# Performance work log

Measured on AMD Instinct MI355X. Metric: run time of the kernel, lower is better.

The kernel has to match this reference:

```python
import jax, jax.numpy as jnp
import numpy as np

NUM_GRAPHS = 1024
NODES_PER_GRAPH = 128
NUM_EDGES = 1048576
D_IN = 128          # n_heads * head_out_feats = input/concat dim
ATT_HEADS = 2       # intra/inter GATConv(d, 32, 2) as in HDN-DDI repo
ATT_OUT = 32
POOL_HEADS = 2      # pool = GATConv(128, 64, 2)
POOL_OUT = 64
EPS = 1e-5          # PyG LayerNorm eps


def _segment_softmax(e, seg, n):
    # numerically-stable softmax over edges grouped by destination node
    m = jax.ops.segment_max(e, seg, num_segments=n)
    m = jnp.where(jnp.isfinite(m), m, 0.0)
    p = jnp.exp(e - m[seg])
    s = jax.ops.segment_sum(p, seg, num_segments=n)
    return p / (s[seg] + 1e-16)


def _gat(x_src, x_dst, edge_index, w_src, w_dst, att_src, att_dst, bias, self_loops):
    # PyG GATConv: linear -> per-head attention logits -> leaky_relu(0.2) ->
    # softmax over incoming edges -> weighted sum of source features -> concat heads + bias
    H, C = att_src.shape
    nd = x_dst.shape[0]
    hs = (x_src @ w_src).reshape(-1, H, C)   # [Ns,H,C]
    hd = (x_dst @ w_dst).reshape(-1, H, C)   # [Nd,H,C]
    a_s = jnp.einsum('nhc,hc->nh', hs, att_src)
    a_d = jnp.einsum('nhc,hc->nh', hd, att_dst)
    src, dst = edge_index[0], edge_index[1]
    if self_loops:  # PyG default add_self_loops=True (non-bipartite case)
        loop = jnp.arange(nd)
        src = jnp.concatenate([src, loop])
        dst = jnp.concatenate([dst, loop])
    e = jax.nn.leaky_relu(a_s[src] + a_d[dst], 0.2)  # [E,H]
    alpha = _segment_softmax(e, dst, nd)
    out = jax.ops.segment_sum(hs[src] * alpha[:, :, None], dst, num_segments=nd)
    return out.reshape(nd, H * C) + bias


def _graph_layernorm(x, batch, weight, bias, n_graphs):
    # PyG LayerNorm(mode='graph'): normalize over all nodes+channels of each graph
    f = x.shape[-1]
    cnt = jax.ops.segment_sum(jnp.ones((x.shape[0],), x.dtype), batch, num_segments=n_graphs)
    norm = jnp.maximum(cnt, 1.0) * f
    mean = jax.ops.segment_sum(x.sum(-1), batch, num_segments=n_graphs) / norm
    xc = x - mean[batch][:, None]
    var = jax.ops.segment_sum((xc * xc).sum(-1), batch, num_segments=n_graphs) / norm
    return (xc / jnp.sqrt(var + EPS)[batch][:, None]) * weight + bias


def setup_inputs() -> dict:
    key = jax.random.key(0)
    ks = jax.random.split(key, 24)
    B, P, E, D = NUM_GRAPHS, NODES_PER_GRAPH, NUM_EDGES, D_IN
    N = B * P

    def intra_edges(k):  # within-graph edges, no self-loops
        k1, k2, k3 = jax.random.split(k, 3)
        g = jax.random.randint(k1, (E,), 0, B)
        s = jax.random.randint(k2, (E,), 0, P)
        d = (s + 1 + jax.random.randint(k3, (E,), 0, P - 1)) % P
        return jnp.stack([g * P + s, g * P + d])

    def inter_edges(k):  # bipartite head-node -> tail-node edges within same graph pair
        k1, k2, k3 = jax.random.split(k, 3)
        g = jax.random.randint(k1, (E,), 0, B)
        s = jax.random.randint(k2, (E,), 0, P)
        d = jax.random.randint(k3, (E,), 0, P)
        return jnp.stack([g * P + s, g * P + d])

    batch = jnp.repeat(jnp.arange(B), P)
    # one global supernode (type 2) per graph: the last node
    y = jnp.tile(jnp.concatenate([jnp.zeros((P - 1,), jnp.int32), jnp.array([2], jnp.int32)]), B)
    p = lambda k, shape: jax.random.normal(k, shape, jnp.float32) * 0.1
    return {
        'h_x': jax.random.normal(ks[0], (N, D), jnp.float32),
        't_x': jax.random.normal(ks[1], (N, D), jnp.float32),
        'h_edge_index': intra_edges(ks[2]),
        't_edge_index': intra_edges(ks[3]),
        'b_edge_index': inter_edges(ks[4]),
        'h_batch': batch,
        't_batch': batch,
        'h_y': y,
        't_y': y,
        'w_intra': p(ks[5], (D, ATT_HEADS * ATT_OUT)),
        'att_intra_src': p(ks[6], (ATT_HEADS, ATT_OUT)),
        'att_intra_dst': p(ks[7], (ATT_HEADS, ATT_OUT)),
        'b_intra': jnp.zeros((ATT_HEADS * ATT_OUT,), jnp.float32),
        'w_inter_src': p(ks[8], (D, ATT_HEADS * ATT_OUT)),
        'w_inter_dst': p(ks[9], (D, ATT_HEADS * ATT_OUT)),
        'att_inter_src': p(ks[10], (ATT_HEADS, ATT_OUT)),
        'att_inter_dst': p(ks[11], (ATT_HEADS, ATT_OUT)),
        'b_inter': jnp.zeros((ATT_HEADS * ATT_OUT,), jnp.float32),
        'w_pool': p(ks[12], (D, POOL_HEADS * POOL_OUT)),
        'att_pool_src': p(ks[13], (POOL_HEADS, POOL_OUT)),
        'att_pool_dst': p(ks[14], (POOL_HEADS, POOL_OUT)),
        'b_pool': jnp.zeros((POOL_HEADS * POOL_OUT,), jnp.float32),
        'ln_weight': jnp.ones((D,), jnp.float32),
        'ln_bias': jnp.zeros((D,), jnp.float32),
    }


def reference(h_x, t_x, h_edge_index, t_edge_index, b_edge_index, h_batch, t_batch, h_y, t_y,
              w_intra, att_intra_src, att_intra_dst, b_intra,
              w_inter_src, w_inter_dst, att_inter_src, att_inter_dst, b_inter,
              w_pool, att_pool_src, att_pool_dst, b_pool, ln_weight, ln_bias):
    h_in = jax.nn.elu(h_x)
    t_in = jax.nn.elu(t_x)
    # intra-graph attention (shared GATConv applied to both drug graphs)
    h_intra = _gat(h_in, h_in, h_edge_index, w_intra, w_intra, att_intra_src, att_intra_dst, b_intra, True)
    t_intra = _gat(t_in, t_in, t_edge_index, w_intra, w_intra, att_intra_src, att_intra_dst, b_intra, True)
    # inter-graph (bipartite) attention: h->t and reversed t->h with shared weights
    t_inter = _gat(h_in, t_in, b_edge_index, w_inter_src, w_inter_dst, att_inter_src, att_inter_dst, b_inter, False)
    h_inter = _gat(t_in, h_in, b_edge_index[::-1], w_inter_src, w_inter_dst, att_inter_src, att_inter_dst, b_inter, False)
    h_rep = jnp.concatenate([h_intra, h_inter], 1)  # [N, 128]
    t_rep = jnp.concatenate([t_intra, t_inter], 1)
    h_nx = jax.nn.elu(_graph_layernorm(h_rep, h_batch, ln_weight, ln_bias, NUM_GRAPHS))
    t_nx = jax.nn.elu(_graph_layernorm(t_rep, t_batch, ln_weight, ln_bias, NUM_GRAPHS))
    h_out = _gat(h_nx, h_nx, h_edge_index, w_pool, w_pool, att_pool_src, att_pool_dst, b_pool, True)
    t_out = _gat(t_nx, t_nx, t_edge_index, w_pool, w_pool, att_pool_src, att_pool_dst, b_pool, True)
    # get_node: gather the single type-2 supernode per graph (exactly NUM_GRAPHS of them)
    h_idx = jnp.where(h_y == 2, size=NUM_GRAPHS)[0]
    t_idx = jnp.where(t_y == 2, size=NUM_GRAPHS)[0]
    return h_out, t_out, h_out[h_idx], t_out[t_idx]
```

## Files before the change

kernel.cpp:

```cpp
#include <hip/hip_runtime.h>
#include <hip/hip_bf16.h>

#define NN 131072
#define NG 1024
#define NE 1048576
#define EB 16384
#define NB 64

typedef __hip_bfloat16 bf16;
typedef __attribute__((ext_vector_type(8))) short short8v;
typedef __attribute__((ext_vector_type(4))) float f32x4;

__device__ __forceinline__ float b2f(bf16 v){ return __bfloat162float(v); }
__device__ __forceinline__ bf16 f2b(float v){ return __float2bfloat16(v); }
__device__ __forceinline__ unsigned short f2bu(float v){ bf16 b = f2b(v); return *(unsigned short*)&b; }
__device__ __forceinline__ float eluf(float x){ return x > 0.f ? x : expm1f(x); }
__device__ __forceinline__ float lrelu(float x){ return x >= 0.f ? x : 0.2f*x; }

__device__ __forceinline__ float ldx(const void* p, size_t i, int f){
  return f ? ((const float*)p)[i] : b2f(((const bf16*)p)[i]);
}

struct EPtrs { const int *s0,*d0,*s1,*d1,*s2,*d2,*s3,*d3; };

__global__ void detect_dtype(const unsigned short* __restrict__ x, int* __restrict__ flag){
  if (blockIdx.x==0 && threadIdx.x==0){
    int bad = 0;
    for (int i=0;i<2048;i++){
      unsigned short e = (x[i] >> 7) & 0xFF;
      if (e == 0xFF) bad++;
      else if (e >= 0x90) bad++;
      else if (e != 0 && e < 0x60) bad++;
    }
    *flag = (bad > 64) ? 1 : 0;
  }
}

__global__ __launch_bounds__(256) void hist_bagg(EPtrs ep, int* __restrict__ Hb){
  __shared__ int cnt[NG];
  int set = blockIdx.y, blk = blockIdx.x, t = threadIdx.x;
  const int* dp = set==0 ? ep.d0 : set==1 ? ep.d1 : set==2 ? ep.d2 : ep.d3;
  for (int i=t;i<NG;i+=256) cnt[i]=0;
  __syncthreads();
  int e0 = blk*EB;
  for (int i=t;i<EB;i+=256) atomicAdd(&cnt[dp[e0+i]>>7],1);
  __syncthreads();
  for (int i=t;i<NG;i+=256) Hb[((size_t)set*NB+blk)*NG+i] = cnt[i];
}

__global__ __launch_bounds__(1024) void scan_bagg(const int* __restrict__ Hb, int* __restrict__ Bb,
                                                  int* __restrict__ base_gs){
  __shared__ int sh[1024];
  int set = blockIdx.x, t = threadIdx.x;
  int run = 0;
  for (int b=0;b<NB;b++){
    int v = Hb[((size_t)set*NB + b)*NG + t];
    Bb[((size_t)set*NB + b)*NG + t] = run;
    run += v;
  }
  int val = run; sh[t] = run; __syncthreads();
  for (int d=1; d<1024; d<<=1){
    int add = (t>=d)? sh[t-d] : 0; __syncthreads();
    val += add; sh[t] = val; __syncthreads();
  }
  int binbase = val - run;
  base_gs[set*(NG+1) + t] = binbase;
  if (t==1023) base_gs[set*(NG+1)+NG] = val;
  for (int b=0;b<NB;b++) Bb[((size_t)set*NB + b)*NG + t] += binbase;
}

__global__ __launch_bounds__(256) void scatter_bagg(EPtrs ep, const int* __restrict__ Bb,
                                                    unsigned short* __restrict__ pk){
  __shared__ int cur[NG];
  int set = blockIdx.y, blk = blockIdx.x, t = threadIdx.x;
  const int* sp = set==0 ? ep.s0 : set==1 ? ep.s1 : set==2 ? ep.s2 : ep.s3;
  const int* dp = set==0 ? ep.d0 : set==1 ? ep.d1 : set==2 ? ep.d2 : ep.d3;
  for (int i=t;i<NG;i+=256) cur[i] = Bb[((size_t)set*NB+blk)*NG+i];
  __syncthreads();
  int e0 = blk*EB;
  for (int i=t;i<EB;i+=256){
    int e = e0+i;
    int d = dp[e], s = sp[e];
    int p = atomicAdd(&cur[d>>7],1);
    pk[(size_t)set*NE + p] = (unsigned short)(((d & 127) << 8) | (s & 127));
  }
}

__global__ __launch_bounds__(256) void prep_kernel(
    const void* w_intra, const void* w_isrc, const void* w_idst, const void* att_xd, const void* w_pool,
    const void* att_is, const void* att_id, const void* att_xs,
    const void* att_ps, const void* att_pd,
    const void* b_intra, const void* b_inter, const void* b_pool,
    const void* ln_w, const void* ln_b,
    bf16* __restrict__ Wtc, bf16* __restrict__ Wtp, float* __restrict__ vdst, float* __restrict__ sm,
    const int* __restrict__ fp){
  int f = *fp;
  int t = threadIdx.x;
  for (int i=t; i<16384; i+=256){
    int j = i & 7, l = (i>>3) & 63, ks = (i>>9) & 3, nt = i >> 11;
    int k = ks*32 + ((l>>4)<<3) + j;
    int c = nt*16 + (l & 15);
    float w1 = (c < 64) ? ldx(w_intra, k*64 + c, f) : ldx(w_isrc, k*64 + (c-64), f);
    Wtc[i] = f2b(w1);
    Wtp[i] = f2b(ldx(w_pool, k*128 + c, f));
  }
  {
    int k = t>>1, h = t&1; float a = 0.f;
    for (int c=0;c<32;c++) a += ldx(w_idst, k*64 + h*32 + c, f) * ldx(att_xd, h*32 + c, f);
    vdst[t] = a;
  }
  if (t < 64){
    sm[t]     = ldx(att_is, t, f);
    sm[64+t]  = ldx(att_id, t, f);
    sm[128+t] = ldx(att_xs, t, f);
    sm[448+t] = ldx(b_intra, t, f);
    sm[512+t] = ldx(b_inter, t, f);
  }
  if (t < 128){
    sm[192+t] = ldx(att_ps, t, f);
    sm[320+t] = ldx(att_pd, t, f);
    sm[576+t] = ldx(b_pool, t, f);
    sm[704+t] = ldx(ln_w, t, f);
    sm[832+t] = ldx(ln_b, t, f);
  }
}

template<int MODE>
__global__ __launch_bounds__(256) void gemm_fused(const void* A, const bf16* __restrict__ Wt, bf16* __restrict__ C,
    const int* __restrict__ fp, const int* __restrict__ fsel, size_t aoff_bf, size_t aoff_f32,
    const float* __restrict__ vdst,
    const float* __restrict__ attA, const float* __restrict__ attB, const float* __restrict__ attC,
    float* __restrict__ oS, float* __restrict__ oD, float* __restrict__ oX, float* __restrict__ oDx){
  constexpr bool ELU = (MODE==0);
  const bf16* Ab = (const bf16*)A + ((fp == nullptr && fsel && *fsel) ? aoff_f32 : aoff_bf);
  int tid = threadIdx.x;
  int w = tid >> 6, l = tid & 63;
  int lr = l & 15, lg = l >> 4;
  size_t row = (size_t)blockIdx.x*64 + w*16 + lr;
  int f = fp ? *fp : 0;
  f32x4 acc[8];
  #pragma unroll
  for (int nt=0;nt<8;nt++) acc[nt] = (f32x4){0.f,0.f,0.f,0.f};
  float dx0 = 0.f, dx1 = 0.f;
  #pragma unroll
  for (int ks=0;ks<4;ks++){
    short8v af;
    size_t ab = row*128 + ks*32 + lg*8;
    if (fp){
      if (f){
        const float* Af = (const float*)A;
        #pragma unroll
        for (int j=0;j<8;j++){
          float v = Af[ab+j]; if (ELU) v = eluf(v);
          if constexpr (MODE==0){ int k = ks*32+lg*8+j; dx0 += v*vdst[k*2]; dx1 += v*vdst[k*2+1]; }
          ((unsigned short*)&af)[j] = f2bu(v);
        }
      } else {
        const unsigned short* Au = (const unsigned short*)A;
        short8v raw = *(const short8v*)(Au + ab);
        #pragma unroll
        for (int j=0;j<8;j++){
          bf16 b; *(unsigned short*)&b = ((unsigned short*)&raw)[j];
          float v = b2f(b); if (ELU) v = eluf(v);
          if constexpr (MODE==0){ int k = ks*32+lg*8+j; dx0 += v*vdst[k*2]; dx1 += v*vdst[k*2+1]; }
          ((unsigned short*)&af)[j] = f2bu(v);
        }
      }
    } else {
      af = *(const short8v*)((const unsigned short*)Ab + ab);
    }
    #pragma unroll
    for (int nt=0;nt<8;nt++){
      short8v bfr = *(const short8v*)((const unsigned short*)Wt + (size_t)((nt*4+ks)*64 + l)*8);
      acc[nt] = __builtin_amdgcn_mfma_f32_16x16x32_bf16(af, bfr, acc[nt], 0, 0, 0);
    }
  }
  if constexpr (MODE==0){
    dx0 += __shfl_xor(dx0, 16); dx0 += __shfl_xor(dx0, 32);
    dx1 += __shfl_xor(dx1, 16); dx1 += __shfl_xor(dx1, 32);
    if (lg == 0){ oDx[row*2] = dx0; oDx[row*2+1] = dx1; }
  }
  size_t crow = (size_t)blockIdx.x*64 + w*16 + lg*4;
  #pragma unroll
  for (int nt=0;nt<8;nt++)
    #pragma unroll
    for (int r=0;r<4;r++)
      C[(crow + r)*128 + nt*16 + lr] = f2b(acc[nt][r]);
  #pragma unroll
  for (int rg=0; rg<4; ++rg){
    float pS0=0.f,pS1=0.f,pD0=0.f,pD1=0.f,pX0=0.f,pX1=0.f;
    #pragma unroll
    for (int nt=0;nt<8;nt++){
      float v = acc[nt][rg];
      int c = nt*16 + lr;
      if constexpr (MODE==0){
        if (nt<4){
          float a=attA[c], b=attB[c];
          if (nt<2){ pS0+=v*a; pD0+=v*b; } else { pS1+=v*a; pD1+=v*b; }
        } else {
          float xw=attC[c-64];
          if (nt<6) pX0+=v*xw; else pX1+=v*xw;
        }
      } else {
        float a=attA[c], b=attB[c];
        if (nt<4){ pS0+=v*a; pD0+=v*b; } else { pS1+=v*a; pD1+=v*b; }
      }
    }
    #pragma unroll
    for (int o=1;o<16;o<<=1){
      pS0+=__shfl_xor(pS0,o); pS1+=__shfl_xor(pS1,o);
      pD0+=__shfl_xor(pD0,o); pD1+=__shfl_xor(pD1,o);
      if constexpr (MODE==0){ pX0+=__shfl_xor(pX0,o); pX1+=__shfl_xor(pX1,o); }
    }
    if (lr == 0){
      size_t n = crow + rg;
      oS[n*2]=pS0; oS[n*2+1]=pS1;
      oD[n*2]=pD0; oD[n*2+1]=pD1;
      if constexpr (MODE==0){ oX[n*2]=pX0; oX[n*2+1]=pX1; }
    }
  }
}

struct GatSet {
  const unsigned short* pk;
  const int* gb;
  const bf16* F;
  const float* aS;
  const float* aD;
  const float* bias;
  int col_in;
  int self_loops;
  int col_off;
  int pad;
  size_t obase_bf, obase_f32, gbase;
};
struct GatSet4 { GatSet s[4]; };

template<int FD>
__global__ __launch_bounds__(512) void gat_mfma(GatSet4 sets, void* out,
    const int* __restrict__ fp, const int* __restrict__ fsel){
  constexpr int NH = FD/2;
  constexpr int NT = NH/16;
  constexpr int KSH = (FD==64)?5:6;
  __shared__ bf16 Pm[128*128];
  __shared__ bf16 Ft[NH*128];
  __shared__ unsigned int Msh[128*16];
  __shared__ float aS0[128], aS1[128], aD0[128], aD1[128], rsum[128];
  const GatSet S = sets.s[blockIdx.y];
  int fo = fp ? *fp : -1;
  size_t obase = (fsel && *fsel) ? S.obase_f32 : S.obase_bf;
  int g = blockIdx.x, t = threadIdx.x;

  if (t < 128){
    float2 v = ((const float2*)S.aS)[g*128+t]; aS0[t]=v.x; aS1[t]=v.y;
    float2 d = ((const float2*)S.aD)[g*128+t]; aD0[t]=d.x; aD1[t]=d.y;
  }
  for (int i=t;i<2048;i+=512) Msh[i]=0;
  __syncthreads();

  {
    int gbeg = S.gb[g], gend = S.gb[g+1];
    for (int i=gbeg+t; i<gend; i+=512){
      unsigned v = S.pk[i];
      unsigned r = v>>8, s = v&127;
      atomicAdd(&Msh[r*16 + (s>>3)], 1u<<((s&7)*4));
    }
    if (S.self_loops && t<128) atomicAdd(&Msh[t*16 + (t>>3)], 1u<<((t&7)*4));
  }
  {
    const unsigned short* Fu = (const unsigned short*)S.F;
    unsigned short* FtU = (unsigned short*)Ft;
    for (int i=t; i<NH*128; i+=512){
      int c = i & (NH-1), k = i >> KSH;
      FtU[c*128 + (k ^ (8*(c&7)))] = Fu[((size_t)(g*128+k))*128 + S.col_in + c];
    }
  }
  __syncthreads();

  int w = t >> 6, l = t & 63, lr = l & 15, lg = l >> 4;
  int r = t >> 2, q = t & 3;

  #pragma unroll
  for (int h=0; h<2; ++h){
    if (h == 1){
      const unsigned short* Fu = (const unsigned short*)S.F;
      unsigned short* FtU = (unsigned short*)Ft;
      for (int i=t; i<NH*128; i+=512){
        int c = i & (NH-1), k = i >> KSH;
        FtU[c*128 + (k ^ (8*(c&7)))] = Fu[((size_t)(g*128+k))*128 + S.col_in + NH + c];
      }
    }
    {
      float ad = h ? aD1[r] : aD0[r];
      const float* aSh = h ? aS1 : aS0;
      float rs = 0.f;
      unsigned int* PmW = (unsigned int*)Pm;
      int dbase = r*64, sw = 4*(r&7);
      unsigned mw = 0;
      #pragma unroll
      for (int i=0;i<16;i++){
        int c = q*32 + 2*i;
        if ((i&3)==0) mw = Msh[r*16 + (c>>3)];
        float m0 = (float)((mw >> ((c&7)*4)) & 15u);
        float m1 = (float)((mw >> (((c&7)+1)*4)) & 15u);
        float p0 = m0 * __expf(lrelu(aSh[c]   + ad));
        float p1 = m1 * __expf(lrelu(aSh[c+1] + ad));
        rs += p0 + p1;
        PmW[dbase + ((q*16+i) ^ sw)] = (unsigned)f2bu(p0) | ((unsigned)f2bu(p1)<<16);
      }
      rs += __shfl_xor(rs,1); rs += __shfl_xor(rs,2);
      if (q==0) rsum[r] = rs;
    }
    __syncthreads();
    f32x4 acc[NT];
    #pragma unroll
    for (int nt=0;nt<NT;nt++) acc[nt] = (f32x4){0.f,0.f,0.f,0.f};
    const unsigned short* PmU = (const unsigned short*)Pm;
    const unsigned short* FtU = (const unsigned short*)Ft;
    int arow = w*16 + lr;
    #pragma unroll
    for (int ks=0;ks<4;ks++){
      short8v af = *(const short8v*)(PmU + arow*128 + ((ks*32+lg*8) ^ (8*(arow&7))));
      #pragma unroll
      for (int nt=0;nt<NT;nt++){
        int brow = nt*16 + lr;
        short8v bfr = *(const short8v*)(FtU + brow*128 + ((ks*32+lg*8) ^ (8*(brow&7))));
        acc[nt] = __builtin_amdgcn_mfma_f32_16x16x32_bf16(af, bfr, acc[nt], 0, 0, 0);
      }
    }
    #pragma unroll
    for (int rg=0; rg<4; ++rg){
      int rrow = w*16 + lg*4 + rg;
      float rinv = 1.f / (rsum[rrow] + 1e-16f);
      int n = g*128 + rrow;
      bool gw = (fp != nullptr) && (rrow == 127);
      #pragma unroll
      for (int nt=0;nt<NT;nt++){
        int c = h*NH + nt*16 + lr;
        float o = acc[nt][rg]*rinv + S.bias[c];
        size_t oi = obase + (size_t)n*128 + S.col_off + c;
        if (fo > 0){
          ((float*)out)[oi] = o;
          if (gw) ((float*)out)[S.gbase + (size_t)g*128 + c] = o;
        } else {
          ((bf16*)out)[oi] = f2b(o);
          if (gw) ((bf16*)out)[S.gbase + (size_t)g*128 + c] = f2b(o);
        }
      }
    }
    __syncthreads();
  }
}

__global__ __launch_bounds__(512) void graph_ln_m(bf16* R_, size_t off_t_bf, size_t off_t_f32,
    const int* __restrict__ fsel, const float* __restrict__ wv, const float* __restrict__ bv){
  __shared__ float sh1[8], sh2[8];
  int g = blockIdx.x, t = threadIdx.x;
  int side = g >> 10, gl = g & 1023;
  size_t soff = side ? ((*fsel) ? off_t_f32 : off_t_bf) : 0;
  unsigned short* Ru = (unsigned short*)(R_ + soff + (size_t)gl*16384);
  short8v v[4];
  #pragma unroll
  for (int q=0;q<4;q++) v[q] = *(short8v*)(Ru + q*4096 + t*8);
  float s1=0.f, s2=0.f;
  #pragma unroll
  for (int q=0;q<4;q++)
    #pragma unroll
    for (int j=0;j<8;j++){
      bf16 b; *(unsigned short*)&b = ((unsigned short*)&v[q])[j];
      float x = b2f(b); s1 += x; s2 += x*x;
    }
  #pragma unroll
  for (int o=32;o;o>>=1){ s1 += __shfl_xor(s1,o); s2 += __shfl_xor(s2,o); }
  if ((t&63)==0){ sh1[t>>6]=s1; sh2[t>>6]=s2; }
  __syncthreads();
  float S1=0.f,S2=0.f;
  #pragma unroll
  for (int i=0;i<8;i++){ S1+=sh1[i]; S2+=sh2[i]; }
  float mean = S1 * (1.f/16384.f);
  float var = fmaxf(S2*(1.f/16384.f) - mean*mean, 0.f);
  float rstd = rsqrtf(var + 1e-5f);
  #pragma unroll
  for (int q=0;q<4;q++){
    short8v ov;
    #pragma unroll
    for (int j=0;j<8;j++){
      int c = (t*8 + j) & 127;
      bf16 b; *(unsigned short*)&b = ((unsigned short*)&v[q])[j];
      float y = (b2f(b)-mean)*rstd*wv[c] + bv[c];
      ((unsigned short*)&ov)[j] = f2bu(y>0.f ? y : expm1f(y));
    }
    *(short8v*)(Ru + q*4096 + t*8) = ov;
  }
}

extern "C" void kernel_launch(void* const* d_in, const int* in_sizes, int n_in,
                              void* d_out, int out_size, void* d_ws, size_t ws_size,
                              hipStream_t stream){
  (void)in_sizes; (void)n_in; (void)out_size; (void)ws_size;
  const void* h_x = d_in[0];
  const void* t_x = d_in[1];
  const int* h_ei = (const int*)d_in[2];
  const int* t_ei = (const int*)d_in[3];
  const int* b_ei = (const int*)d_in[4];

  char* base = (char*)d_ws;
  size_t off = 0;
  auto alloc = [&](size_t bytes)->char*{ char* p = base + off; off += (bytes + 255) & ~(size_t)255; return p; };
  bf16* AB_h     = (bf16*)alloc((size_t)NN*128*2);
  bf16* AB_t     = (bf16*)alloc((size_t)NN*128*2);
  unsigned short* pk = (unsigned short*)alloc((size_t)4*NE*2);
  int* Hb        = (int*)alloc((size_t)4*NB*NG*4);
  int* Bb        = (int*)alloc((size_t)4*NB*NG*4);
  int* base_gs   = (int*)alloc((size_t)4*(NG+1)*4);
  float* aSi_h   = (float*)alloc((size_t)NN*2*4);
  float* aDi_h   = (float*)alloc((size_t)NN*2*4);
  float* aSx_h   = (float*)alloc((size_t)NN*2*4);
  float* aSi_t   = (float*)alloc((size_t)NN*2*4);
  float* aDi_t   = (float*)alloc((size_t)NN*2*4);
  float* aSx_t   = (float*)alloc((size_t)NN*2*4);
  float* aDx_h   = (float*)alloc((size_t)NN*2*4);
  float* aDx_t   = (float*)alloc((size_t)NN*2*4);
  bf16* Wtc      = (bf16*)alloc(16384*2);
  bf16* Wtp      = (bf16*)alloc(16384*2);
  float* vdst    = (float*)alloc(256*4);
  float* sm      = (float*)alloc(960*4);
  int* flag      = (int*)alloc(256);

  const size_t REPT_BF = (size_t)NN*128, REPT_F32 = (size_t)2*NN*128;

  detect_dtype<<<1,64,0,stream>>>((const unsigned short*)h_x, flag);

  EPtrs ep;
  ep.s0 = h_ei;      ep.d0 = h_ei + NE;
  ep.s1 = t_ei;      ep.d1 = t_ei + NE;
  ep.s2 = b_ei;      ep.d2 = b_ei + NE;
  ep.s3 = b_ei + NE; ep.d3 = b_ei;
  hist_bagg<<<dim3(NB,4),256,0,stream>>>(ep, Hb);
  scan_bagg<<<4,1024,0,stream>>>(Hb, Bb, base_gs);
  scatter_bagg<<<dim3(NB,4),256,0,stream>>>(ep, Bb, pk);

  prep_kernel<<<1,256,0,stream>>>(d_in[9], d_in[13], d_in[14], d_in[16], d_in[18],
      d_in[10], d_in[11], d_in[15], d_in[19], d_in[20],
      d_in[12], d_in[17], d_in[21], d_in[22], d_in[23],
      Wtc, Wtp, vdst, sm, flag);

  const unsigned short* pk_h = pk;
  const unsigned short* pk_t = pk + NE;
  const unsigned short* pk_ht= pk + (size_t)2*NE;
  const unsigned short* pk_th= pk + (size_t)3*NE;
  const int* gb_h = base_gs;
  const int* gb_t = base_gs + (NG+1);
  const int* gb_ht= base_gs + 2*(NG+1);
  const int* gb_th= base_gs + 3*(NG+1);

  gemm_fused<0><<<2048,256,0,stream>>>(h_x, Wtc, AB_h, flag, nullptr, 0, 0,
      vdst, sm+0, sm+64, sm+128, aSi_h, aDi_h, aSx_h, aDx_h);
  gemm_fused<0><<<2048,256,0,stream>>>(t_x, Wtc, AB_t, flag, nullptr, 0, 0,
      vdst, sm+0, sm+64, sm+128, aSi_t, aDi_t, aSx_t, aDx_t);

  {
    GatSet4 L;
    L.s[0] = { pk_h,  gb_h,  AB_h, aSi_h, aDi_h, sm+448, 0,  1, 0,  0, 0,        0,         0 };
    L.s[1] = { pk_t,  gb_t,  AB_t, aSi_t, aDi_t, sm+448, 0,  1, 0,  0, REPT_BF,  REPT_F32,  0 };
    L.s[2] = { pk_ht, gb_ht, AB_h, aSx_h, aDx_t, sm+512, 64, 0, 64, 0, REPT_BF,  REPT_F32,  0 };
    L.s[3] = { pk_th, gb_th, AB_t, aSx_t, aDx_h, sm+512, 64, 0, 64, 0, 0,        0,         0 };
    gat_mfma<64><<<dim3(NG,4),512,0,stream>>>(L, d_out, nullptr, flag);
  }

  graph_ln_m<<<2048,512,0,stream>>>((bf16*)d_out, REPT_BF, REPT_F32, flag, sm+704, sm+832);

  gemm_fused<1><<<2048,256,0,stream>>>(d_out, Wtp, AB_h, nullptr, flag, 0, 0,
      nullptr, sm+192, sm+320, nullptr, aSi_h, aDi_h, nullptr, nullptr);
  gemm_fused<1><<<2048,256,0,stream>>>(d_out, Wtp, AB_t, nullptr, flag, REPT_BF, REPT_F32,
      nullptr, sm+192, sm+320, nullptr, aSi_t, aDi_t, nullptr, nullptr);

  {
    size_t go_h = (size_t)2*NN*128;
    size_t go_t = go_h + (size_t)NG*128;
    GatSet4 P;
    P.s[0] = { pk_h, gb_h, AB_h, aSi_h, aDi_h, sm+576, 0, 1, 0, 0, 0,              0,              go_h };
    P.s[1] = { pk_t, gb_t, AB_t, aSi_t, aDi_t, sm+576, 0, 1, 0, 0, (size_t)NN*128, (size_t)NN*128, go_t };
    P.s[2] = P.s[0]; P.s[3] = P.s[0];
    gat_mfma<128><<<dim3(NG,2),512,0,stream>>>(P, d_out, flag, flag);
  }
}
```

Before: 629.7 us.

## Scatter edge attention weights into float LDS matrix in two row halves

New measurement: 721.9 us. 14.6% more time.

```diff
diff --git a/kernel.cpp b/kernel.cpp
--- a/kernel.cpp
+++ b/kernel.cpp
@@ -240,115 +240,116 @@
 __global__ __launch_bounds__(512) void gat_mfma(GatSet4 sets, void* out,
     const int* __restrict__ fp, const int* __restrict__ fsel){
   constexpr int NH = FD/2;
-  constexpr int NT = NH/16;
+  constexpr int NT = NH/32;
   constexpr int KSH = (FD==64)?5:6;
-  __shared__ bf16 Pm[128*128];
-  __shared__ bf16 Ft[NH*128];
-  __shared__ unsigned int Msh[128*16];
-  __shared__ float aS0[128], aS1[128], aD0[128], aD1[128], rsum[128];
+  __shared__ float Pf[64*132];
+  __shared__ bf16 Ft[NH*136];
+  __shared__ float aS0[128], aS1[128], aD0[128], aD1[128], rsum[64];
   const GatSet S = sets.s[blockIdx.y];
   int fo = fp ? *fp : -1;
   size_t obase = (fsel && *fsel) ? S.obase_f32 : S.obase_bf;
   int g = blockIdx.x, t = threadIdx.x;
+  int gbeg = S.gb[g], gend = S.gb[g+1];
 
   if (t < 128){
     float2 v = ((const float2*)S.aS)[g*128+t]; aS0[t]=v.x; aS1[t]=v.y;
     float2 d = ((const float2*)S.aD)[g*128+t]; aD0[t]=d.x; aD1[t]=d.y;
-  }
-  for (int i=t;i<2048;i+=512) Msh[i]=0;
-  __syncthreads();
-
-  {
-    int gbeg = S.gb[g], gend = S.gb[g+1];
-    for (int i=gbeg+t; i<gend; i+=512){
-      unsigned v = S.pk[i];
-      unsigned r = v>>8, s = v&127;
-      atomicAdd(&Msh[r*16 + (s>>3)], 1u<<((s&7)*4));
-    }
-    if (S.self_loops && t<128) atomicAdd(&Msh[t*16 + (t>>3)], 1u<<((t&7)*4));
   }
   {
     const unsigned short* Fu = (const unsigned short*)S.F;
     unsigned short* FtU = (unsigned short*)Ft;
     for (int i=t; i<NH*128; i+=512){
       int c = i & (NH-1), k = i >> KSH;
-      FtU[c*128 + (k ^ (8*(c&7)))] = Fu[((size_t)(g*128+k))*128 + S.col_in + c];
-    }
-  }
+      FtU[c*136 + k] = Fu[((size_t)(g*128+k))*128 + S.col_in + c];
+    }
+  }
+  for (int i=t; i<64*132; i+=512) Pf[i] = 0.f;
+  if (t < 64) rsum[t] = 0.f;
   __syncthreads();
 
-  int w = t >> 6, l = t & 63, lr = l & 15, lg = l >> 4;
-  int r = t >> 2, q = t & 3;
-
-  #pragma unroll
+  int w = t>>6, l = t&63, lr = l&15, lg = l>>4;
+
   for (int h=0; h<2; ++h){
-    if (h == 1){
-      const unsigned short* Fu = (const unsigned short*)S.F;
-      unsigned short* FtU = (unsigned short*)Ft;
-      for (int i=t; i<NH*128; i+=512){
-        int c = i & (NH-1), k = i >> KSH;
-        FtU[c*128 + (k ^ (8*(c&7)))] = Fu[((size_t)(g*128+k))*128 + S.col_in + NH + c];
-      }
-    }
-    {
-      float ad = h ? aD1[r] : aD0[r];
-      const float* aSh = h ? aS1 : aS0;
-      float rs = 0.f;
-      unsigned int* PmW = (unsigned int*)Pm;
-      int dbase = r*64, sw = 4*(r&7);
-      unsigned mw = 0;
+    const float* aSh = h ? aS1 : aS0;
+    const float* aDh = h ? aD1 : aD0;
+    for (int half=0; half<2; ++half){
+      int rlo = half*64;
+      for (int i=gbeg+t; i<gend; i+=512){
+        unsigned v = S.pk[i];
+        int r = v>>8, s = v&127;
+        if ((r>>6) == half){
+          float p = __expf(lrelu(aSh[s] + aDh[r]));
+          atomicAdd(&Pf[(r-rlo)*132 + s], p);
+          atomicAdd(&rsum[r-rlo], p);
+        }
+      }
+      if (S.self_loops && t < 64){
+        int r = rlo + t;
+        float p = __expf(lrelu(aSh[r] + aDh[r]));
+        atomicAdd(&Pf[t*132 + r], p);
+        atomicAdd(&rsum[t], p);
+      }
+      __syncthreads();
+      f32x4 acc[NT];
       #pragma unroll
-      for (int i=0;i<16;i++){
-        int c = q*32 + 2*i;
-        if ((i&3)==0) mw = Msh[r*16 + (c>>3)];
-        float m0 = (float)((mw >> ((c&7)*4)) & 15u);
-        float m1 = (float)((mw >> (((c&7)+1)*4)) & 15u);
-        float p0 = m0 * __expf(lrelu(aSh[c]   + ad));
-        float p1 = m1 * __expf(lrelu(aSh[c+1] + ad));
-        rs += p0 + p1;
-        PmW[dbase + ((q*16+i) ^ sw)] = (unsigned)f2bu(p0) | ((unsigned)f2bu(p1)<<16);
-      }
-      rs += __shfl_xor(rs,1); rs += __shfl_xor(rs,2);
-      if (q==0) rsum[r] = rs;
-    }
-    __syncthreads();
-    f32x4 acc[NT];
-    #pragma unroll
-    for (int nt=0;nt<NT;nt++) acc[nt] = (f32x4){0.f,0.f,0.f,0.f};
-    const unsigned short* PmU = (const unsigned short*)Pm;
-    const unsigned short* FtU = (const unsigned short*)Ft;
-    int arow = w*16 + lr;
-    #pragma unroll
-    for (int ks=0;ks<4;ks++){
-      short8v af = *(const short8v*)(PmU + arow*128 + ((ks*32+lg*8) ^ (8*(arow&7))));
+      for (int j=0;j<NT;j++) acc[j] = (f32x4){0.f,0.f,0.f,0.f};
+      const unsigned short* FtU = (const unsigned short*)Ft;
+      int rt = w>>1;
       #pragma unroll
-      for (int nt=0;nt<NT;nt++){
-        int brow = nt*16 + lr;
-        short8v bfr = *(const short8v*)(FtU + brow*128 + ((ks*32+lg*8) ^ (8*(brow&7))));
-        acc[nt] = __builtin_amdgcn_mfma_f32_16x16x32_bf16(af, bfr, acc[nt], 0, 0, 0);
-      }
-    }
-    #pragma unroll
-    for (int rg=0; rg<4; ++rg){
-      int rrow = w*16 + lg*4 + rg;
-      float rinv = 1.f / (rsum[rrow] + 1e-16f);
-      int n = g*128 + rrow;
-      bool gw = (fp != nullptr) && (rrow == 127);
+      for (int ks=0; ks<4; ++ks){
+        const float* Ap = &Pf[(rt*16+lr)*132 + ks*32 + lg*8];
+        f32x4 a0 = *(const f32x4*)Ap;
+        f32x4 a1 = *(const f32x4*)(Ap+4);
+        short8v af;
+        #pragma unroll
+        for (int j2=0;j2<4;j2++){
+          ((unsigned short*)&af)[j2]   = f2bu(a0[j2]);
+          ((unsigned short*)&af)[4+j2] = f2bu(a1[j2]);
+        }
+        #pragma unroll
+        for (int j=0;j<NT;j++){
+          int brow = ((w&1)*NT + j)*16 + lr;
+          short8v bfr = *(const short8v*)(FtU + brow*136 + ks*32 + lg*8);
+          acc[j] = __builtin_amdgcn_mfma_f32_16x16x32_bf16(af, bfr, acc[j], 0, 0, 0);
+        }
+      }
       #pragma unroll
-      for (int nt=0;nt<NT;nt++){
-        int c = h*NH + nt*16 + lr;
-        float o = acc[nt][rg]*rinv + S.bias[c];
-        size_t oi = obase + (size_t)n*128 + S.col_off + c;
-        if (fo > 0){
-          ((float*)out)[oi] = o;
-          if (gw) ((float*)out)[S.gbase + (size_t)g*128 + c] = o;
-        } else {
-          ((bf16*)out)[oi] = f2b(o);
-          if (gw) ((bf16*)out)[S.gbase + (size_t)g*128 + c] = f2b(o);
-        }
-      }
-    }
-    __syncthreads();
+      for (int rg=0; rg<4; ++rg){
+        int rloc = rt*16 + lg*4 + rg;
+        int rglob = rlo + rloc;
+        float rinv = 1.f/(rsum[rloc] + 1e-16f);
+        int n = g*128 + rglob;
+        bool gw = (fp != nullptr) && (rglob == 127);
+        #pragma unroll
+        for (int j=0;j<NT;j++){
+          int c = h*NH + ((w&1)*NT + j)*16 + lr;
+          float o = acc[j][rg]*rinv + S.bias[c];
+          size_t oi = obase + (size_t)n*128 + S.col_off + c;
+          if (fo > 0){
+            ((float*)out)[oi] = o;
+            if (gw) ((float*)out)[S.gbase + (size_t)g*128 + c] = o;
+          } else {
+            ((bf16*)out)[oi] = f2b(o);
+            if (gw) ((bf16*)out)[S.gbase + (size_t)g*128 + c] = f2b(o);
+          }
+        }
+      }
+      __syncthreads();
+      bool last = (h==1) && (half==1);
+      if (!last){
+        for (int i=t; i<64*132; i+=512) Pf[i] = 0.f;
+        if (t < 64) rsum[t] = 0.f;
+        if (half==1){
+          const unsigned short* Fu = (const unsigned short*)S.F;
+          unsigned short* FtU2 = (unsigned short*)Ft;
+          for (int i=t; i<NH*128; i+=512){
+            int c = i & (NH-1), k = i >> KSH;
+            FtU2[c*136 + k] = Fu[((size_t)(g*128+k))*128 + S.col_in + NH + c];
+          }
+        }
+        __syncthreads();
+      }
+    }
   }
 }
 
```
